# Performance work log

Measured on AMD Instinct MI355X. Metric: run time of the kernel, lower is better.

Reference implementation:

```python
import jax, jax.numpy as jnp
import numpy as np

B, N = 2, 65536
V, VSUB, J, R = 6890, 689, 24, 64
THRESH = 0.12


def trilinear(grid, coords):
    # grid: [C, D, H, W]; coords: [..., 3] in [-1, 1] (x->W, y->H, z->D)
    C, D, H, W = grid.shape
    cs = jnp.clip(coords.reshape(-1, 3), -1.0, 1.0)
    x = (cs[:, 0] + 1.0) * 0.5 * (W - 1)
    y = (cs[:, 1] + 1.0) * 0.5 * (H - 1)
    z = (cs[:, 2] + 1.0) * 0.5 * (D - 1)
    x0 = jnp.floor(x).astype(jnp.int32); x1 = jnp.minimum(x0 + 1, W - 1)
    y0 = jnp.floor(y).astype(jnp.int32); y1 = jnp.minimum(y0 + 1, H - 1)
    z0 = jnp.floor(z).astype(jnp.int32); z1 = jnp.minimum(z0 + 1, D - 1)
    fx = x - x0; fy = y - y0; fz = z - z0
    g = lambda zi, yi, xi: grid[:, zi, yi, xi]  # [C, M]
    out = (g(z0, y0, x0) * ((1 - fz) * (1 - fy) * (1 - fx))
         + g(z0, y0, x1) * ((1 - fz) * (1 - fy) * fx)
         + g(z0, y1, x0) * ((1 - fz) * fy * (1 - fx))
         + g(z0, y1, x1) * ((1 - fz) * fy * fx)
         + g(z1, y0, x0) * (fz * (1 - fy) * (1 - fx))
         + g(z1, y0, x1) * (fz * (1 - fy) * fx)
         + g(z1, y1, x0) * (fz * fy * (1 - fx))
         + g(z1, y1, x1) * (fz * fy * fx))
    return out.T.reshape(coords.shape[:-1] + (C,))


def setup_inputs() -> dict:
    key = jax.random.key(0)
    ks = jax.random.split(key, 8)
    pts_in = jax.random.normal(ks[0], (B, N, 3), jnp.float32) * 0.4
    vs_template = jax.random.normal(ks[1], (1, VSUB, 3), jnp.float32) * 0.4
    shape_offset = jax.random.normal(ks[2], (1, V, 3), jnp.float32) * 0.01
    init_idx = jax.random.randint(ks[3], (N, 3), 0, V, jnp.int32)
    bar = jax.random.uniform(ks[4], (N, 3), jnp.float32) + 1e-3
    init_bar = bar / jnp.sum(bar, -1, keepdims=True)
    lbs_voxel = jax.nn.softmax(jax.random.normal(ks[5], (J, R, R, R), jnp.float32), axis=0)
    tfs = jnp.tile(jnp.eye(4, dtype=jnp.float32), (B, J, 1, 1)) \
        + 0.05 * jax.random.normal(ks[6], (B, J, 4, 4), jnp.float32)
    grid_scale = jnp.full((3,), 1.5, jnp.float32)
    grid_offset = jnp.zeros((3,), jnp.float32)
    return dict(pts_in=pts_in, vs_template=vs_template, shape_offset=shape_offset,
                init_idx=init_idx, init_bar=init_bar, lbs_voxel=lbs_voxel,
                tfs=tfs, grid_scale=grid_scale, grid_offset=grid_offset)


def reference(pts_in, vs_template, shape_offset, init_idx, init_bar, lbs_voxel, tfs, grid_scale, grid_offset):
    # --- KNN (K=1) against subsampled template vertices ---
    v = vs_template[0]  # [VSUB, 3]
    d2 = (jnp.sum(pts_in * pts_in, -1, keepdims=True)
          + jnp.sum(v * v, -1)[None, None, :]
          - 2.0 * jnp.einsum('bnd,vd->bnv', pts_in, v))  # [B,N,VSUB]
    dist_sq = jnp.min(d2, axis=-1)  # [B,N]
    mask = (dist_sq < THRESH ** 2)[..., None]  # [B,N,1]
    # --- barycentric interpolation of per-vertex shape offsets ---
    tri = shape_offset[0][init_idx]               # [N,3,3]
    off = jnp.sum(init_bar[..., None] * tri, -2)  # [N,3]
    pts = pts_in + off[None]
    # --- query LBS weights from explicit voxel grid (fast-SNARF) ---
    pts_norm = (pts - grid_offset) * grid_scale
    w = trilinear(lbs_voxel, pts_norm)  # [B,N,J]
    w = w / jnp.clip(jnp.sum(w, -1, keepdims=True), 1e-6, None)
    # --- forward skinning ---
    w_tf = jnp.einsum('bnj,bjkl->bnkl', w, tfs)  # [B,N,4,4]
    pts_h = jnp.concatenate([pts, jnp.ones_like(pts[..., :1])], -1)  # [B,N,4]
    pts_posed = jnp.einsum('bnkl,bnl->bnk', w_tf, pts_h)[..., :3]
    pts_cano_all = pts_posed.reshape(B, N, 1, 3)
    return pts_cano_all, mask, w_tf
```

## Files before the change

kernel.cpp:

```cpp
#include <hip/hip_runtime.h>
#include <math.h>

#define NB    2
#define NPTS  65536
#define NVSUB 689
#define NJ    24
#define GR    64
#define GRV   (GR*GR*GR)
#define THRESH2 0.0144f

#define O_PTS  0
#define O_MASK (NB*NPTS*3)
#define O_WTF  (O_MASK + NB*NPTS)

__global__ __launch_bounds__(256) void prep_kernel(const float* __restrict__ g,
                                                   float* __restrict__ gt) {
    int vox = blockIdx.x * 256 + threadIdx.x;
    float v[NJ];
#pragma unroll
    for (int c = 0; c < NJ; ++c) v[c] = g[c * GRV + vox];
    float4* dst = (float4*)(gt + (size_t)vox * NJ);
#pragma unroll
    for (int c4 = 0; c4 < 6; ++c4)
        dst[c4] = make_float4(v[4*c4+0], v[4*c4+1], v[4*c4+2], v[4*c4+3]);
}

__global__ __launch_bounds__(256) void mask_kernel(const float* __restrict__ pts_in,
                                                   const float* __restrict__ vs,
                                                   float* __restrict__ out) {
    __shared__ float4 s_vs[NVSUB];
    const int tid = threadIdx.x;
    for (int i = tid; i < NVSUB; i += 256) {
        float x = vs[i * 3 + 0], y = vs[i * 3 + 1], z = vs[i * 3 + 2];
        s_vs[i] = make_float4(x, y, z, x * x + y * y + z * z);
    }
    __syncthreads();

    const int t  = blockIdx.x * 256 + tid;
    const int p  = t >> 2;
    const int qq = t & 3;
    const int b  = p >> 16;
    const int n  = p & (NPTS - 1);

    const float* P = pts_in + ((size_t)b * NPTS + n) * 3;
    const float px = P[0], py = P[1], pz = P[2];

    const int vbeg = qq * 173;
    const int vend = min(vbeg + 173, NVSUB);
    float ma = 3.4e38f, mb = 3.4e38f;
    int v = vbeg;
    for (; v + 2 <= vend; v += 2) {
        float4 t0 = s_vs[v];
        float4 t1 = s_vs[v + 1];
        ma = fminf(ma, fmaf(-2.f, px * t0.x + py * t0.y + pz * t0.z, t0.w));
        mb = fminf(mb, fmaf(-2.f, px * t1.x + py * t1.y + pz * t1.z, t1.w));
    }
    if (v < vend) {
        float4 t0 = s_vs[v];
        ma = fminf(ma, fmaf(-2.f, px * t0.x + py * t0.y + pz * t0.z, t0.w));
    }
    float mm = fminf(ma, mb);
    mm = fminf(mm, __shfl_xor(mm, 1));
    mm = fminf(mm, __shfl_xor(mm, 2));
    if (qq == 0) {
        float dist2 = mm + px * px + py * py + pz * pz;
        out[O_MASK + p] = (dist2 < THRESH2) ? 1.f : 0.f;
    }
}

__global__ __launch_bounds__(256) void deform_kernel(
    const float* __restrict__ pts_in,
    const float* __restrict__ shape_off,
    const int*   __restrict__ init_idx,
    const float* __restrict__ init_bar,
    const float* __restrict__ gT,
    const float* __restrict__ tfs,
    const float* __restrict__ gscale,
    const float* __restrict__ goff,
    float* __restrict__ out) {
    __shared__ float s_part[128][20];

    const int tid = threadIdx.x;
    const int pl  = tid & 127;
    const int hf  = tid >> 7;
    const int p   = blockIdx.x * 128 + pl;
    const int b   = p >> 16;
    const int n   = p & (NPTS - 1);

    const float* P = pts_in + ((size_t)b * NPTS + n) * 3;
    const float px = P[0], py = P[1], pz = P[2];

    int i0 = init_idx[n * 3 + 0] * 3;
    int i1 = init_idx[n * 3 + 1] * 3;
    int i2 = init_idx[n * 3 + 2] * 3;
    float b0 = init_bar[n * 3 + 0], b1 = init_bar[n * 3 + 1], b2 = init_bar[n * 3 + 2];
    float qx = px + b0 * shape_off[i0 + 0] + b1 * shape_off[i1 + 0] + b2 * shape_off[i2 + 0];
    float qy = py + b0 * shape_off[i0 + 1] + b1 * shape_off[i1 + 1] + b2 * shape_off[i2 + 1];
    float qz = pz + b0 * shape_off[i0 + 2] + b1 * shape_off[i1 + 2] + b2 * shape_off[i2 + 2];

    float ccx = fminf(fmaxf((qx - goff[0]) * gscale[0], -1.f), 1.f);
    float ccy = fminf(fmaxf((qy - goff[1]) * gscale[1], -1.f), 1.f);
    float ccz = fminf(fmaxf((qz - goff[2]) * gscale[2], -1.f), 1.f);
    float x = (ccx + 1.f) * 0.5f * (GR - 1);
    float y = (ccy + 1.f) * 0.5f * (GR - 1);
    float z = (ccz + 1.f) * 0.5f * (GR - 1);
    int x0 = (int)floorf(x), y0 = (int)floorf(y), z0 = (int)floorf(z);
    int x1 = min(x0 + 1, GR - 1), y1 = min(y0 + 1, GR - 1), z1 = min(z0 + 1, GR - 1);
    float fx = x - (float)x0, fy = y - (float)y0, fz = z - (float)z0;
    float wxa[2] = {1.f - fx, fx}, wya[2] = {1.f - fy, fy}, wza[2] = {1.f - fz, fz};

    float w[12];
#pragma unroll
    for (int c = 0; c < 12; ++c) w[c] = 0.f;

#pragma unroll
    for (int ci = 0; ci < 8; ++ci) {
        int xi = (ci & 1) ? x1 : x0;
        int yi = (ci & 2) ? y1 : y0;
        int zi = (ci & 4) ? z1 : z0;
        float wt = wxa[ci & 1] * wya[(ci >> 1) & 1] * wza[(ci >> 2) & 1];
        int vox = (zi * GR + yi) * GR + xi;
        const float4* g4 = (const float4*)(gT + (size_t)vox * NJ + hf * 12);
        float4 g0 = g4[0], g1 = g4[1], g2 = g4[2];
        w[0]  = fmaf(wt, g0.x, w[0]);  w[1]  = fmaf(wt, g0.y, w[1]);
        w[2]  = fmaf(wt, g0.z, w[2]);  w[3]  = fmaf(wt, g0.w, w[3]);
        w[4]  = fmaf(wt, g1.x, w[4]);  w[5]  = fmaf(wt, g1.y, w[5]);
        w[6]  = fmaf(wt, g1.z, w[6]);  w[7]  = fmaf(wt, g1.w, w[7]);
        w[8]  = fmaf(wt, g2.x, w[8]);  w[9]  = fmaf(wt, g2.y, w[9]);
        w[10] = fmaf(wt, g2.z, w[10]); w[11] = fmaf(wt, g2.w, w[11]);
    }
    float wsum = 0.f;
#pragma unroll
    for (int c = 0; c < 12; ++c) wsum += w[c];

    const int bu  = __builtin_amdgcn_readfirstlane(b);
    const int hfu = __builtin_amdgcn_readfirstlane(hf);
    const float* tb = tfs + (size_t)(bu * NJ + hfu * 12) * 16;
    float acc[16];
#pragma unroll
    for (int k = 0; k < 16; ++k) acc[k] = 0.f;
#pragma unroll
    for (int jj = 0; jj < 12; ++jj) {
        float wj = w[jj];
#pragma unroll
        for (int k = 0; k < 16; ++k) acc[k] = fmaf(wj, tb[jj * 16 + k], acc[k]);
    }

    if (hf == 1) {
        float* sp = &s_part[pl][0];
        ((float4*)sp)[0] = make_float4(acc[0],  acc[1],  acc[2],  acc[3]);
        ((float4*)sp)[1] = make_float4(acc[4],  acc[5],  acc[6],  acc[7]);
        ((float4*)sp)[2] = make_float4(acc[8],  acc[9],  acc[10], acc[11]);
        ((float4*)sp)[3] = make_float4(acc[12], acc[13], acc[14], acc[15]);
        sp[16] = wsum;
    }
    __syncthreads();

    if (hf == 0) {
        const float* sp = &s_part[pl][0];
        float4 q0 = ((const float4*)sp)[0], q1 = ((const float4*)sp)[1];
        float4 q2 = ((const float4*)sp)[2], q3 = ((const float4*)sp)[3];
        acc[0] += q0.x;  acc[1] += q0.y;  acc[2] += q0.z;  acc[3] += q0.w;
        acc[4] += q1.x;  acc[5] += q1.y;  acc[6] += q1.z;  acc[7] += q1.w;
        acc[8] += q2.x;  acc[9] += q2.y;  acc[10] += q2.z; acc[11] += q2.w;
        acc[12] += q3.x; acc[13] += q3.y; acc[14] += q3.z; acc[15] += q3.w;
        wsum += sp[16];
        float inv = __builtin_amdgcn_rcpf(fmaxf(wsum, 1e-6f));
#pragma unroll
        for (int k = 0; k < 16; ++k) acc[k] *= inv;

        float ox = acc[0] * qx + acc[1] * qy + acc[2]  * qz + acc[3];
        float oy = acc[4] * qx + acc[5] * qy + acc[6]  * qz + acc[7];
        float oz = acc[8] * qx + acc[9] * qy + acc[10] * qz + acc[11];

        size_t bn = (size_t)p;
        out[O_PTS + bn * 3 + 0] = ox;
        out[O_PTS + bn * 3 + 1] = oy;
        out[O_PTS + bn * 3 + 2] = oz;
        float4* wt4 = (float4*)(out + O_WTF + bn * 16);
        wt4[0] = make_float4(acc[0],  acc[1],  acc[2],  acc[3]);
        wt4[1] = make_float4(acc[4],  acc[5],  acc[6],  acc[7]);
        wt4[2] = make_float4(acc[8],  acc[9],  acc[10], acc[11]);
        wt4[3] = make_float4(acc[12], acc[13], acc[14], acc[15]);
    }
}

__global__ __launch_bounds__(256) void snarf_fallback(
    const float* __restrict__ pts_in, const float* __restrict__ vs,
    const float* __restrict__ shape_off, const int* __restrict__ init_idx,
    const float* __restrict__ init_bar, const float* __restrict__ grid,
    const float* __restrict__ tfs, const float* __restrict__ gscale,
    const float* __restrict__ goff, float* __restrict__ out) {
    const int n = blockIdx.x * 256 + threadIdx.x;
    for (int b = 0; b < NB; ++b) {
        float px = pts_in[((size_t)b * NPTS + n) * 3 + 0];
        float py = pts_in[((size_t)b * NPTS + n) * 3 + 1];
        float pz = pts_in[((size_t)b * NPTS + n) * 3 + 2];
        float mm = 3.4e38f;
        for (int v = 0; v < NVSUB; ++v) {
            float dx = px - vs[v * 3 + 0], dy = py - vs[v * 3 + 1], dz = pz - vs[v * 3 + 2];
            mm = fminf(mm, dx * dx + dy * dy + dz * dz);
        }
        int i0 = init_idx[n * 3 + 0] * 3, i1 = init_idx[n * 3 + 1] * 3, i2 = init_idx[n * 3 + 2] * 3;
        float b0 = init_bar[n * 3 + 0], b1 = init_bar[n * 3 + 1], b2 = init_bar[n * 3 + 2];
        float qx = px + b0 * shape_off[i0 + 0] + b1 * shape_off[i1 + 0] + b2 * shape_off[i2 + 0];
        float qy = py + b0 * shape_off[i0 + 1] + b1 * shape_off[i1 + 1] + b2 * shape_off[i2 + 1];
        float qz = pz + b0 * shape_off[i0 + 2] + b1 * shape_off[i1 + 2] + b2 * shape_off[i2 + 2];
        float cx = fminf(fmaxf((qx - goff[0]) * gscale[0], -1.f), 1.f);
        float cy = fminf(fmaxf((qy - goff[1]) * gscale[1], -1.f), 1.f);
        float cz = fminf(fmaxf((qz - goff[2]) * gscale[2], -1.f), 1.f);
        float x = (cx + 1.f) * 0.5f * (GR - 1), y = (cy + 1.f) * 0.5f * (GR - 1), z = (cz + 1.f) * 0.5f * (GR - 1);
        int x0 = (int)floorf(x), y0 = (int)floorf(y), z0 = (int)floorf(z);
        int x1 = min(x0 + 1, GR - 1), y1 = min(y0 + 1, GR - 1), z1 = min(z0 + 1, GR - 1);
        float fx = x - x0, fy = y - y0, fz = z - z0;
        float wxa[2] = {1.f - fx, fx}, wya[2] = {1.f - fy, fy}, wza[2] = {1.f - fz, fz};
        float w[NJ];
        for (int c = 0; c < NJ; ++c) w[c] = 0.f;
        for (int ci = 0; ci < 8; ++ci) {
            int xi = (ci & 1) ? x1 : x0, yi = (ci & 2) ? y1 : y0, zi = (ci & 4) ? z1 : z0;
            float wt = wxa[ci & 1] * wya[(ci >> 1) & 1] * wza[(ci >> 2) & 1];
            int vox = (zi * GR + yi) * GR + xi;
            for (int c = 0; c < NJ; ++c) w[c] = fmaf(wt, grid[c * GRV + vox], w[c]);
        }
        float s = 0.f;
        for (int c = 0; c < NJ; ++c) s += w[c];
        float inv = 1.f / fmaxf(s, 1e-6f);
        float acc[16];
        for (int k = 0; k < 16; ++k) acc[k] = 0.f;
        for (int j = 0; j < NJ; ++j) {
            float wj = w[j] * inv;
            for (int k = 0; k < 16; ++k) acc[k] = fmaf(wj, tfs[(b * NJ + j) * 16 + k], acc[k]);
        }
        size_t bn = (size_t)b * NPTS + n;
        out[O_PTS + bn * 3 + 0] = acc[0] * qx + acc[1] * qy + acc[2] * qz + acc[3];
        out[O_PTS + bn * 3 + 1] = acc[4] * qx + acc[5] * qy + acc[6] * qz + acc[7];
        out[O_PTS + bn * 3 + 2] = acc[8] * qx + acc[9] * qy + acc[10] * qz + acc[11];
        out[O_MASK + bn] = (mm < THRESH2) ? 1.f : 0.f;
        for (int k = 0; k < 16; ++k) out[O_WTF + bn * 16 + k] = acc[k];
    }
}

extern "C" void kernel_launch(void* const* d_in, const int* in_sizes, int n_in,
                              void* d_out, int out_size, void* d_ws, size_t ws_size,
                              hipStream_t stream) {
    const float* pts_in    = (const float*)d_in[0];
    const float* vs        = (const float*)d_in[1];
    const float* shape_off = (const float*)d_in[2];
    const int*   init_idx  = (const int*)d_in[3];
    const float* init_bar  = (const float*)d_in[4];
    const float* lbs       = (const float*)d_in[5];
    const float* tfs       = (const float*)d_in[6];
    const float* gs        = (const float*)d_in[7];
    const float* go        = (const float*)d_in[8];
    float* out = (float*)d_out;

    const size_t needed = (size_t)GRV * NJ * sizeof(float);
    if (ws_size >= needed) {
        float* gT = (float*)d_ws;
        prep_kernel<<<GRV / 256, 256, 0, stream>>>(lbs, gT);
        mask_kernel<<<(NB * NPTS * 4) / 256, 256, 0, stream>>>(pts_in, vs, out);
        deform_kernel<<<(NB * NPTS) / 128, 256, 0, stream>>>(
            pts_in, shape_off, init_idx, init_bar, gT, tfs, gs, go, out);
    } else {
        snarf_fallback<<<NPTS / 256, 256, 0, stream>>>(
            pts_in, vs, shape_off, init_idx, init_bar, lbs, tfs, gs, go, out);
    }
}
```

Before: 151.0 us.

## Merge prep and mask kernels; split deform joints across four lanes with shuffle reduce

The grid transpose and KNN mask kernels are merged into one launch by partitioning block indices, which removes one launch and lets the two independent workloads overlap. The deform kernel now assigns four lanes per point, each handling six joints, and reduces the partial 4x4 matrices with warp shuffles instead of a two-half shared-memory exchange. Transforms are staged in shared memory and launch bounds request higher occupancy. This trades more redundant per-point setup (index loads, trilinear coordinates) and shuffle traffic for more parallelism and smaller per-thread register state.

```diff
diff --git a/kernel.cpp b/kernel.cpp
--- a/kernel.cpp
+++ b/kernel.cpp
@@ -13,30 +13,35 @@
 #define O_MASK (NB*NPTS*3)
 #define O_WTF  (O_MASK + NB*NPTS)
 
-__global__ __launch_bounds__(256) void prep_kernel(const float* __restrict__ g,
-                                                   float* __restrict__ gt) {
-    int vox = blockIdx.x * 256 + threadIdx.x;
-    float v[NJ];
-#pragma unroll
-    for (int c = 0; c < NJ; ++c) v[c] = g[c * GRV + vox];
-    float4* dst = (float4*)(gt + (size_t)vox * NJ);
-#pragma unroll
-    for (int c4 = 0; c4 < 6; ++c4)
-        dst[c4] = make_float4(v[4*c4+0], v[4*c4+1], v[4*c4+2], v[4*c4+3]);
-}
-
-__global__ __launch_bounds__(256) void mask_kernel(const float* __restrict__ pts_in,
-                                                   const float* __restrict__ vs,
-                                                   float* __restrict__ out) {
+#define PREP_BLOCKS (GRV / 256)
+#define MASK_BLOCKS ((NB * NPTS * 4) / 256)
+
+__global__ __launch_bounds__(256) void prep_mask_kernel(
+    const float* __restrict__ g, float* __restrict__ gt,
+    const float* __restrict__ pts_in, const float* __restrict__ vs,
+    float* __restrict__ out) {
     __shared__ float4 s_vs[NVSUB];
     const int tid = threadIdx.x;
+
+    if (blockIdx.x < PREP_BLOCKS) {
+        int vox = blockIdx.x * 256 + tid;
+        float v[NJ];
+#pragma unroll
+        for (int c = 0; c < NJ; ++c) v[c] = g[c * GRV + vox];
+        float4* dst = (float4*)(gt + (size_t)vox * NJ);
+#pragma unroll
+        for (int c4 = 0; c4 < 6; ++c4)
+            dst[c4] = make_float4(v[4*c4+0], v[4*c4+1], v[4*c4+2], v[4*c4+3]);
+        return;
+    }
+
     for (int i = tid; i < NVSUB; i += 256) {
         float x = vs[i * 3 + 0], y = vs[i * 3 + 1], z = vs[i * 3 + 2];
         s_vs[i] = make_float4(x, y, z, x * x + y * y + z * z);
     }
     __syncthreads();
 
-    const int t  = blockIdx.x * 256 + tid;
+    const int t  = (blockIdx.x - PREP_BLOCKS) * 256 + tid;
     const int p  = t >> 2;
     const int qq = t & 3;
     const int b  = p >> 16;
@@ -68,7 +73,7 @@
     }
 }
 
-__global__ __launch_bounds__(256) void deform_kernel(
+__global__ __launch_bounds__(256, 6) void deform_kernel(
     const float* __restrict__ pts_in,
     const float* __restrict__ shape_off,
     const int*   __restrict__ init_idx,
@@ -78,14 +83,17 @@
     const float* __restrict__ gscale,
     const float* __restrict__ goff,
     float* __restrict__ out) {
-    __shared__ float s_part[128][20];
+    __shared__ float s_tfs[NB * NJ * 16];
 
     const int tid = threadIdx.x;
-    const int pl  = tid & 127;
-    const int hf  = tid >> 7;
-    const int p   = blockIdx.x * 128 + pl;
-    const int b   = p >> 16;
-    const int n   = p & (NPTS - 1);
+    for (int i = tid; i < NB * NJ * 16; i += 256) s_tfs[i] = tfs[i];
+    __syncthreads();
+
+    const int t = blockIdx.x * 256 + tid;
+    const int p = t >> 2;
+    const int q = t & 3;
+    const int b = p >> 16;
+    const int n = p & (NPTS - 1);
 
     const float* P = pts_in + ((size_t)b * NPTS + n) * 3;
     const float px = P[0], py = P[1], pz = P[2];
@@ -109,9 +117,9 @@
     float fx = x - (float)x0, fy = y - (float)y0, fz = z - (float)z0;
     float wxa[2] = {1.f - fx, fx}, wya[2] = {1.f - fy, fy}, wza[2] = {1.f - fz, fz};
 
-    float w[12];
-#pragma unroll
-    for (int c = 0; c < 12; ++c) w[c] = 0.f;
+    float w[6];
+#pragma unroll
+    for (int c = 0; c < 6; ++c) w[c] = 0.f;
 
 #pragma unroll
     for (int ci = 0; ci < 8; ++ci) {
@@ -120,68 +128,57 @@
         int zi = (ci & 4) ? z1 : z0;
         float wt = wxa[ci & 1] * wya[(ci >> 1) & 1] * wza[(ci >> 2) & 1];
         int vox = (zi * GR + yi) * GR + xi;
-        const float4* g4 = (const float4*)(gT + (size_t)vox * NJ + hf * 12);
-        float4 g0 = g4[0], g1 = g4[1], g2 = g4[2];
-        w[0]  = fmaf(wt, g0.x, w[0]);  w[1]  = fmaf(wt, g0.y, w[1]);
-        w[2]  = fmaf(wt, g0.z, w[2]);  w[3]  = fmaf(wt, g0.w, w[3]);
-        w[4]  = fmaf(wt, g1.x, w[4]);  w[5]  = fmaf(wt, g1.y, w[5]);
-        w[6]  = fmaf(wt, g1.z, w[6]);  w[7]  = fmaf(wt, g1.w, w[7]);
-        w[8]  = fmaf(wt, g2.x, w[8]);  w[9]  = fmaf(wt, g2.y, w[9]);
-        w[10] = fmaf(wt, g2.z, w[10]); w[11] = fmaf(wt, g2.w, w[11]);
-    }
-    float wsum = 0.f;
-#pragma unroll
-    for (int c = 0; c < 12; ++c) wsum += w[c];
-
-    const int bu  = __builtin_amdgcn_readfirstlane(b);
-    const int hfu = __builtin_amdgcn_readfirstlane(hf);
-    const float* tb = tfs + (size_t)(bu * NJ + hfu * 12) * 16;
-    float acc[16];
-#pragma unroll
-    for (int k = 0; k < 16; ++k) acc[k] = 0.f;
-#pragma unroll
-    for (int jj = 0; jj < 12; ++jj) {
+        const float2* g2 = (const float2*)(gT + (size_t)vox * NJ + q * 6);
+        float2 ga = g2[0], gb = g2[1], gc = g2[2];
+        w[0] = fmaf(wt, ga.x, w[0]); w[1] = fmaf(wt, ga.y, w[1]);
+        w[2] = fmaf(wt, gb.x, w[2]); w[3] = fmaf(wt, gb.y, w[3]);
+        w[4] = fmaf(wt, gc.x, w[4]); w[5] = fmaf(wt, gc.y, w[5]);
+    }
+    float wsum = w[0] + w[1] + w[2] + w[3] + w[4] + w[5];
+
+    float4 A0 = make_float4(0.f, 0.f, 0.f, 0.f);
+    float4 A1 = A0, A2 = A0, A3 = A0;
+    const float4* tb = (const float4*)(s_tfs + (size_t)(b * NJ + q * 6) * 16);
+#pragma unroll
+    for (int jj = 0; jj < 6; ++jj) {
         float wj = w[jj];
-#pragma unroll
-        for (int k = 0; k < 16; ++k) acc[k] = fmaf(wj, tb[jj * 16 + k], acc[k]);
-    }
-
-    if (hf == 1) {
-        float* sp = &s_part[pl][0];
-        ((float4*)sp)[0] = make_float4(acc[0],  acc[1],  acc[2],  acc[3]);
-        ((float4*)sp)[1] = make_float4(acc[4],  acc[5],  acc[6],  acc[7]);
-        ((float4*)sp)[2] = make_float4(acc[8],  acc[9],  acc[10], acc[11]);
-        ((float4*)sp)[3] = make_float4(acc[12], acc[13], acc[14], acc[15]);
-        sp[16] = wsum;
-    }
-    __syncthreads();
-
-    if (hf == 0) {
-        const float* sp = &s_part[pl][0];
-        float4 q0 = ((const float4*)sp)[0], q1 = ((const float4*)sp)[1];
-        float4 q2 = ((const float4*)sp)[2], q3 = ((const float4*)sp)[3];
-        acc[0] += q0.x;  acc[1] += q0.y;  acc[2] += q0.z;  acc[3] += q0.w;
-        acc[4] += q1.x;  acc[5] += q1.y;  acc[6] += q1.z;  acc[7] += q1.w;
-        acc[8] += q2.x;  acc[9] += q2.y;  acc[10] += q2.z; acc[11] += q2.w;
-        acc[12] += q3.x; acc[13] += q3.y; acc[14] += q3.z; acc[15] += q3.w;
-        wsum += sp[16];
+        float4 r0 = tb[jj * 4 + 0], r1 = tb[jj * 4 + 1];
+        float4 r2 = tb[jj * 4 + 2], r3 = tb[jj * 4 + 3];
+        A0.x = fmaf(wj, r0.x, A0.x); A0.y = fmaf(wj, r0.y, A0.y);
+        A0.z = fmaf(wj, r0.z, A0.z); A0.w = fmaf(wj, r0.w, A0.w);
+        A1.x = fmaf(wj, r1.x, A1.x); A1.y = fmaf(wj, r1.y, A1.y);
+        A1.z = fmaf(wj, r1.z, A1.z); A1.w = fmaf(wj, r1.w, A1.w);
+        A2.x = fmaf(wj, r2.x, A2.x); A2.y = fmaf(wj, r2.y, A2.y);
+        A2.z = fmaf(wj, r2.z, A2.z); A2.w = fmaf(wj, r2.w, A2.w);
+        A3.x = fmaf(wj, r3.x, A3.x); A3.y = fmaf(wj, r3.y, A3.y);
+        A3.z = fmaf(wj, r3.z, A3.z); A3.w = fmaf(wj, r3.w, A3.w);
+    }
+
+#define QRED(v) v += __shfl_xor(v, 1); v += __shfl_xor(v, 2)
+    QRED(A0.x); QRED(A0.y); QRED(A0.z); QRED(A0.w);
+    QRED(A1.x); QRED(A1.y); QRED(A1.z); QRED(A1.w);
+    QRED(A2.x); QRED(A2.y); QRED(A2.z); QRED(A2.w);
+    QRED(A3.x); QRED(A3.y); QRED(A3.z); QRED(A3.w);
+    QRED(wsum);
+#undef QRED
+
+    if (q == 0) {
         float inv = __builtin_amdgcn_rcpf(fmaxf(wsum, 1e-6f));
-#pragma unroll
-        for (int k = 0; k < 16; ++k) acc[k] *= inv;
-
-        float ox = acc[0] * qx + acc[1] * qy + acc[2]  * qz + acc[3];
-        float oy = acc[4] * qx + acc[5] * qy + acc[6]  * qz + acc[7];
-        float oz = acc[8] * qx + acc[9] * qy + acc[10] * qz + acc[11];
+        A0.x *= inv; A0.y *= inv; A0.z *= inv; A0.w *= inv;
+        A1.x *= inv; A1.y *= inv; A1.z *= inv; A1.w *= inv;
+        A2.x *= inv; A2.y *= inv; A2.z *= inv; A2.w *= inv;
+        A3.x *= inv; A3.y *= inv; A3.z *= inv; A3.w *= inv;
+
+        float ox = A0.x * qx + A0.y * qy + A0.z * qz + A0.w;
+        float oy = A1.x * qx + A1.y * qy + A1.z * qz + A1.w;
+        float oz = A2.x * qx + A2.y * qy + A2.z * qz + A2.w;
 
         size_t bn = (size_t)p;
         out[O_PTS + bn * 3 + 0] = ox;
         out[O_PTS + bn * 3 + 1] = oy;
         out[O_PTS + bn * 3 + 2] = oz;
         float4* wt4 = (float4*)(out + O_WTF + bn * 16);
-        wt4[0] = make_float4(acc[0],  acc[1],  acc[2],  acc[3]);
-        wt4[1] = make_float4(acc[4],  acc[5],  acc[6],  acc[7]);
-        wt4[2] = make_float4(acc[8],  acc[9],  acc[10], acc[11]);
-        wt4[3] = make_float4(acc[12], acc[13], acc[14], acc[15]);
+        wt4[0] = A0; wt4[1] = A1; wt4[2] = A2; wt4[3] = A3;
     }
 }
 
@@ -257,9 +254,9 @@
     const size_t needed = (size_t)GRV * NJ * sizeof(float);
     if (ws_size >= needed) {
         float* gT = (float*)d_ws;
-        prep_kernel<<<GRV / 256, 256, 0, stream>>>(lbs, gT);
-        mask_kernel<<<(NB * NPTS * 4) / 256, 256, 0, stream>>>(pts_in, vs, out);
-        deform_kernel<<<(NB * NPTS) / 128, 256, 0, stream>>>(
+        prep_mask_kernel<<<PREP_BLOCKS + MASK_BLOCKS, 256, 0, stream>>>(
+            lbs, gT, pts_in, vs, out);
+        deform_kernel<<<(NB * NPTS * 4) / 256, 256, 0, stream>>>(
             pts_in, shape_off, init_idx, init_bar, gT, tfs, gs, go, out);
     } else {
         snarf_fallback<<<NPTS / 256, 256, 0, stream>>>(
```

After: 140.1 us. 7.2% less time.
